# Kernel tuning notes

Hardware: AMD Instinct MI355X
Metric: run time of the kernel (lower is better)

## Reference

```python
import jax, jax.numpy as jnp
import numpy as np

B, T, S, U, VOCAB = 32, 64, 64, 512, 65


def setup_inputs() -> dict:
    key = jax.random.key(0)
    ks = jax.random.split(key, 16)
    sd = 0.05
    return {
        "shifted_labels": jax.random.randint(ks[0], (B, T), 0, VOCAB),
        "encoder_output": jax.random.normal(ks[1], (B, S, U), jnp.float32),
        "enc_state_h": jax.random.normal(ks[2], (B, U), jnp.float32),
        "enc_state_c": jax.random.normal(ks[3], (B, U), jnp.float32),
        # decoder LSTM params (keras gate order i,f,g,o)
        "Wx": jax.random.normal(ks[4], (VOCAB, 4 * U), jnp.float32) * sd,
        "Wh": jax.random.normal(ks[5], (U, 4 * U), jnp.float32) * sd,
        "b": jnp.zeros((4 * U,), jnp.float32),
        # Bahdanau attention params
        "W1": jax.random.normal(ks[6], (U, U), jnp.float32) * sd,
        "b1": jnp.zeros((U,), jnp.float32),
        "W2": jax.random.normal(ks[7], (U, U), jnp.float32) * sd,
        "b2": jnp.zeros((U,), jnp.float32),
        "V": jax.random.normal(ks[8], (U, 1), jnp.float32) * sd,
        "bv": jnp.zeros((1,), jnp.float32),
    }


def _lstm(xz, h0, c0, Wh):
    # xz: [B, T, 4U] precomputed input projections
    def step(carry, xz_t):
        h, c = carry
        z = xz_t + h @ Wh
        i, f, g, o = jnp.split(z, 4, axis=-1)
        c = jax.nn.sigmoid(f) * c + jax.nn.sigmoid(i) * jnp.tanh(g)
        h = jax.nn.sigmoid(o) * jnp.tanh(c)
        return (h, c), h

    (_, _), hs = jax.lax.scan(step, (h0, c0), jnp.swapaxes(xz, 0, 1))
    return jnp.swapaxes(hs, 0, 1)  # [B, T, U]


def reference(shifted_labels, encoder_output, enc_state_h, enc_state_c,
              Wx, Wh, b, W1, b1, W2, b2, V, bv):
    vocab = Wx.shape[0]
    x = jax.nn.one_hot(shifted_labels, vocab, dtype=encoder_output.dtype)  # [B,T,vocab]
    xz = jnp.einsum('btv,vk->btk', x, Wx) + b                              # [B,T,4U]
    dec = _lstm(xz, enc_state_h, enc_state_c, Wh)                          # [B,T,U]
    # Bahdanau attention, vectorized over all decoder timesteps at once
    d1 = dec @ W1 + b1                # [B,T,U]
    e2 = encoder_output @ W2 + b2     # [B,S,U]  (computed once, not per step)
    score = jnp.tanh(d1[:, :, None, :] + e2[:, None, :, :]) @ V + bv  # [B,T,S,1]
    w = jax.nn.softmax(score[..., 0], axis=-1)  # softmax over encoder positions S
    return jnp.transpose(w, (0, 2, 1))          # [B,S,T] (stack axis=2 in original)
```

## Files before the change

### kernel.cpp

```cpp
#include <hip/hip_runtime.h>
#include <hip/hip_bf16.h>


#define NB 32
#define NT 64
#define NS 64
#define NU 512
#define N4U 2048
#define NV 65
#define NWG 32

typedef unsigned int u32;
typedef __bf16 bf16_t;
typedef bf16_t bf16x8 __attribute__((ext_vector_type(8)));
typedef float f32x4 __attribute__((ext_vector_type(4)));
typedef u32 u32x4 __attribute__((ext_vector_type(4)));

__device__ __forceinline__ unsigned short f2bf(float f) {
  u32 u = __builtin_bit_cast(u32, f);
  u += 0x7fffu + ((u >> 16) & 1u);
  return (unsigned short)(u >> 16);
}
__device__ __forceinline__ float bf2f(unsigned short s) {
  return __builtin_bit_cast(float, (u32)s << 16);
}
__device__ __forceinline__ u32 pk2(float a, float b) {
  return (u32)f2bf(a) | ((u32)f2bf(b) << 16);
}
__device__ __forceinline__ float sigf(float x) { return 1.0f / (1.0f + __expf(-x)); }
__device__ __forceinline__ float tanhfast(float x) {
  float e = __expf(2.0f * x);
  return 1.0f - 2.0f / (e + 1.0f);
}

#define LOAD_HSLOT(DST, AP)                                                   \
  asm volatile(                                                               \
    "global_load_dwordx4 %0, %16, off sc0 sc1\n\t"                            \
    "global_load_dwordx4 %1, %16, off offset:64 sc0 sc1\n\t"                  \
    "global_load_dwordx4 %2, %16, off offset:128 sc0 sc1\n\t"                 \
    "global_load_dwordx4 %3, %16, off offset:192 sc0 sc1\n\t"                 \
    "global_load_dwordx4 %4, %16, off offset:256 sc0 sc1\n\t"                 \
    "global_load_dwordx4 %5, %16, off offset:320 sc0 sc1\n\t"                 \
    "global_load_dwordx4 %6, %16, off offset:384 sc0 sc1\n\t"                 \
    "global_load_dwordx4 %7, %16, off offset:448 sc0 sc1\n\t"                 \
    "global_load_dwordx4 %8, %16, off offset:512 sc0 sc1\n\t"                 \
    "global_load_dwordx4 %9, %16, off offset:576 sc0 sc1\n\t"                 \
    "global_load_dwordx4 %10, %16, off offset:640 sc0 sc1\n\t"                \
    "global_load_dwordx4 %11, %16, off offset:704 sc0 sc1\n\t"                \
    "global_load_dwordx4 %12, %16, off offset:768 sc0 sc1\n\t"                \
    "global_load_dwordx4 %13, %16, off offset:832 sc0 sc1\n\t"                \
    "global_load_dwordx4 %14, %16, off offset:896 sc0 sc1\n\t"                \
    "global_load_dwordx4 %15, %16, off offset:960 sc0 sc1\n\t"                \
    "s_waitcnt vmcnt(0)"                                                      \
    : "=&v"(DST[0]),  "=&v"(DST[1]),  "=&v"(DST[2]),  "=&v"(DST[3]),          \
      "=&v"(DST[4]),  "=&v"(DST[5]),  "=&v"(DST[6]),  "=&v"(DST[7]),          \
      "=&v"(DST[8]),  "=&v"(DST[9]),  "=&v"(DST[10]), "=&v"(DST[11]),         \
      "=&v"(DST[12]), "=&v"(DST[13]), "=&v"(DST[14]), "=&v"(DST[15])          \
    : "v"(AP)                                                                 \
    : "memory")

__global__ __launch_bounds__(256, 1)
void lstm_kernel(const int* __restrict__ labels,
                 const float* __restrict__ h0,
                 const float* __restrict__ c0,
                 const float* __restrict__ Wx,
                 const float* __restrict__ Wh,
                 const float* __restrict__ bias,
                 const float* __restrict__ enc,
                 const float* __restrict__ W2,
                 const float* __restrict__ b2,
                 const float* __restrict__ W1,
                 const float* __restrict__ b1,
                 u32* __restrict__ hbuf,
                 u32* __restrict__ flags,
                 unsigned short* __restrict__ d1_bf,
                 unsigned short* __restrict__ e2_bf)
{
  __shared__ float z_buf[NB][65];
  __shared__ float c_lds[NB][16];
  __shared__ float wx_lds[NV][65];
  __shared__ unsigned char lab_lds[NB * NT];

  const int tid  = threadIdx.x;
  const int g    = blockIdx.x;
  const int wave = tid >> 6, lane = tid & 63;
  const int l15  = lane & 15, l4 = lane >> 4;

  if (g >= NWG) {
    const int k = g - NWG;
    {
      const int r0 = k * 64 + wave * 16;
      const int arowE = r0 + l15;
      u32x4 afragE[16];
#pragma unroll
      for (int kt = 0; kt < 16; ++kt) {
        const float* ep = enc + arowE * NU + kt * 32 + l4 * 8;
        u32x4 t;
        t.x = pk2(ep[0], ep[1]); t.y = pk2(ep[2], ep[3]);
        t.z = pk2(ep[4], ep[5]); t.w = pk2(ep[6], ep[7]);
        afragE[kt] = t;
      }
      for (int cg = 0; cg < 8; ++cg) {
        f32x4 acc[4] = {};
        for (int kt = 0; kt < 16; ++kt) {
          bf16x8 a = __builtin_bit_cast(bf16x8, afragE[kt]);
          int k0 = kt * 32 + l4 * 8;
#pragma unroll
          for (int nt = 0; nt < 4; ++nt) {
            int col = cg * 64 + nt * 16 + l15;
            union { unsigned short us[8]; bf16x8 v; } bu;
#pragma unroll
            for (int e = 0; e < 8; ++e) bu.us[e] = f2bf(W2[(k0 + e) * NU + col]);
            acc[nt] = __builtin_amdgcn_mfma_f32_16x16x32_bf16(a, bu.v, acc[nt], 0, 0, 0);
          }
        }
#pragma unroll
        for (int nt = 0; nt < 4; ++nt) {
          int col = cg * 64 + nt * 16 + l15;
          float bc = b2[col];
#pragma unroll
          for (int ri = 0; ri < 4; ++ri)
            e2_bf[(r0 + l4 * 4 + ri) * NU + col] = f2bf(acc[nt][ri] + bc);
        }
      }
    }

    {
      const int wm = wave >> 1, wn = wave & 1;
      const int col = k * 16 + l15;
      const float bc1 = b1[col];
      bf16x8 bfrag1[16];
#pragma unroll
      for (int kt = 0; kt < 16; ++kt) {
        int kb = kt * 32 + l4 * 8;
        union { unsigned short us[8]; bf16x8 v; } bu;
#pragma unroll
        for (int e = 0; e < 8; ++e) bu.us[e] = f2bf(W1[(kb + e) * NU + col]);
        bfrag1[kt] = bu.v;
      }
      const int arow1 = wm * 16 + l15;
      for (int t = 1 + wn; t <= NT; t += 2) {
        {
          int guard = 0;
          for (;;) {
            u32 f = (u32)t;
            if (lane < NWG)
              f = __hip_atomic_load(flags + lane, __ATOMIC_RELAXED,
                                    __HIP_MEMORY_SCOPE_AGENT);
            if (__all(f >= (u32)t)) break;
            if (++guard > 2000000) break;
            __builtin_amdgcn_s_sleep(2);
          }
        }
        u32x4 hf[16];
        const u32* ap1 = hbuf + (size_t)t * 8192 + arow1 * 256 + l4 * 4;
        LOAD_HSLOT(hf, ap1);
        f32x4 acc = {0.f, 0.f, 0.f, 0.f};
#pragma unroll
        for (int kt = 0; kt < 16; ++kt)
          acc = __builtin_amdgcn_mfma_f32_16x16x32_bf16(
                  __builtin_bit_cast(bf16x8, hf[kt]), bfrag1[kt], acc, 0, 0, 0);
#pragma unroll
        for (int ri = 0; ri < 4; ++ri) {
          int b = wm * 16 + l4 * 4 + ri;
          d1_bf[(b * NT + (t - 1)) * NU + col] = f2bf(acc[ri] + bc1);
        }
      }
    }
    return;
  }

  const int wm = wave >> 1, wn = wave & 1;

  for (int i = tid; i < NV * 64; i += 256) {
    int v = i >> 6, c = i & 63;
    int j = (c >> 4) * NU + g * 16 + (c & 15);
    wx_lds[v][c] = Wx[v * N4U + j] + bias[j];
  }
  for (int i = tid; i < NB * 16; i += 256) {
    int r = i >> 4, u = i & 15;
    c_lds[r][u] = c0[r * NU + g * 16 + u];
  }
  for (int i = tid; i < NB * NT; i += 256) lab_lds[i] = (unsigned char)labels[i];

  bf16x8 bfrag[16][2];
#pragma unroll
  for (int kt = 0; kt < 16; ++kt) {
#pragma unroll
    for (int nt = 0; nt < 2; ++nt) {
      int c = wn * 32 + nt * 16 + l15;
      int j = (c >> 4) * NU + g * 16 + (c & 15);
      int kb = kt * 32 + l4 * 8;
      union { unsigned short us[8]; bf16x8 v; } bu;
#pragma unroll
      for (int e = 0; e < 8; ++e) bu.us[e] = f2bf(Wh[(kb + e) * N4U + j]);
      bfrag[kt][nt] = bu.v;
    }
  }

  const int arow = wm * 16 + l15;
  u32x4 afrag[16];
#pragma unroll
  for (int kt = 0; kt < 16; ++kt) {
    const float* hp = h0 + arow * NU + kt * 32 + l4 * 8;
    u32x4 t;
    t.x = pk2(hp[0], hp[1]); t.y = pk2(hp[2], hp[3]);
    t.z = pk2(hp[4], hp[5]); t.w = pk2(hp[6], hp[7]);
    afrag[kt] = t;
  }

  const int bb = tid >> 3;
  const int u2 = (tid & 7) * 2;
  const int ci = g * 8 + (tid & 7);

  for (int s = 0; s < NT; ++s) {
    f32x4 a00 = {0.f,0.f,0.f,0.f}, a01 = a00, a10 = a00, a11 = a00;
#pragma unroll
    for (int kt = 0; kt < 16; kt += 2) {
      bf16x8 av0 = __builtin_bit_cast(bf16x8, afrag[kt]);
      bf16x8 av1 = __builtin_bit_cast(bf16x8, afrag[kt + 1]);
      a00 = __builtin_amdgcn_mfma_f32_16x16x32_bf16(av0, bfrag[kt][0],     a00, 0, 0, 0);
      a10 = __builtin_amdgcn_mfma_f32_16x16x32_bf16(av0, bfrag[kt][1],     a10, 0, 0, 0);
      a01 = __builtin_amdgcn_mfma_f32_16x16x32_bf16(av1, bfrag[kt + 1][0], a01, 0, 0, 0);
      a11 = __builtin_amdgcn_mfma_f32_16x16x32_bf16(av1, bfrag[kt + 1][1], a11, 0, 0, 0);
    }
    f32x4 acc0 = a00 + a01, acc1 = a10 + a11;

#pragma unroll
    for (int ri = 0; ri < 4; ++ri) {
      z_buf[wm * 16 + l4 * 4 + ri][wn * 32 + l15]      = acc0[ri];
      z_buf[wm * 16 + l4 * 4 + ri][wn * 32 + 16 + l15] = acc1[ri];
    }
    __syncthreads();

    int lab = lab_lds[bb * NT + s];
    float hv[2];
#pragma unroll
    for (int q = 0; q < 2; ++q) {
      int u = u2 + q;
      float zi = z_buf[bb][u]      + wx_lds[lab][u];
      float zf = z_buf[bb][16 + u] + wx_lds[lab][16 + u];
      float zg = z_buf[bb][32 + u] + wx_lds[lab][32 + u];
      float zo = z_buf[bb][48 + u] + wx_lds[lab][48 + u];
      float cc = sigf(zf) * c_lds[bb][u] + sigf(zi) * tanhfast(zg);
      c_lds[bb][u] = cc;
      hv[q] = sigf(zo) * tanhfast(cc);
    }
    u32 pkv = pk2(hv[0], hv[1]);

    __hip_atomic_store(hbuf + (size_t)(s + 1) * 8192 + bb * 256 + ci, pkv,
                       __ATOMIC_RELAXED, __HIP_MEMORY_SCOPE_AGENT);

    asm volatile("s_waitcnt vmcnt(0)" ::: "memory");
    __syncthreads();

    if (tid == 0)
      __hip_atomic_store(flags + g, (u32)(s + 1),
                         __ATOMIC_RELAXED, __HIP_MEMORY_SCOPE_AGENT);

    if (s == NT - 1) break;

    {
      const u32 target = (u32)(s + 1);
      int guard = 0;
      for (;;) {
        u32 f = target;
        if (lane < NWG)
          f = __hip_atomic_load(flags + lane, __ATOMIC_RELAXED,
                                __HIP_MEMORY_SCOPE_AGENT);
        if (__all(f >= target)) break;
        if (++guard > 300000) break;
        __builtin_amdgcn_s_sleep(1);
      }
    }

    {
      const u32* ap = hbuf + (size_t)(s + 1) * 8192 + arow * 256 + l4 * 4;
      LOAD_HSLOT(afrag, ap);
    }
  }
}

__global__ __launch_bounds__(256, 1)
void score_kernel(const unsigned short* __restrict__ d1_bf,
                  const unsigned short* __restrict__ e2_bf,
                  const float* __restrict__ V,
                  float* __restrict__ out)
{
  const int tid = threadIdx.x;
  const int wave = tid >> 6, lane = tid & 63;
  const int p = blockIdx.x * 4 + wave;
  const int bb = p >> 6, t = p & 63;

  union { uint4 q; unsigned short us[8]; } dv;
  dv.q = *reinterpret_cast<const uint4*>(d1_bf + (bb * 64 + t) * NU + lane * 8);
  float d1f[8], Vf[8];
#pragma unroll
  for (int e = 0; e < 8; ++e) { d1f[e] = bf2f(dv.us[e]); Vf[e] = V[lane * 8 + e]; }

  float sc = 0.f;
  for (int s = 0; s < NS; ++s) {
    union { uint4 q; unsigned short us[8]; } ev;
    ev.q = *reinterpret_cast<const uint4*>(e2_bf + (bb * 64 + s) * NU + lane * 8);
    float part = 0.f;
#pragma unroll
    for (int e = 0; e < 8; ++e) part += tanhfast(d1f[e] + bf2f(ev.us[e])) * Vf[e];
#pragma unroll
    for (int o = 32; o > 0; o >>= 1) part += __shfl_xor(part, o);
    sc = (lane == s) ? part : sc;
  }
  float m = sc;
#pragma unroll
  for (int o = 32; o > 0; o >>= 1) m = fmaxf(m, __shfl_xor(m, o));
  float ex = __expf(sc - m);
  float sum = ex;
#pragma unroll
  for (int o = 32; o > 0; o >>= 1) sum += __shfl_xor(sum, o);
  out[(bb * 64 + lane) * 64 + t] = ex / sum;
}

extern "C" void kernel_launch(void* const* d_in, const int* in_sizes, int n_in,
                              void* d_out, int out_size, void* d_ws, size_t ws_size,
                              hipStream_t stream)
{
  (void)in_sizes; (void)n_in; (void)out_size;
  const int*   labels = (const int*)  d_in[0];
  const float* enc    = (const float*)d_in[1];
  const float* h0     = (const float*)d_in[2];
  const float* c0     = (const float*)d_in[3];
  const float* Wx     = (const float*)d_in[4];
  const float* Wh     = (const float*)d_in[5];
  const float* bias   = (const float*)d_in[6];
  const float* W1     = (const float*)d_in[7];
  const float* b1     = (const float*)d_in[8];
  const float* W2     = (const float*)d_in[9];
  const float* b2     = (const float*)d_in[10];
  const float* V      = (const float*)d_in[11];

  char* ws = (char*)d_ws;
  const size_t OFS_HB  = 32768;
  const size_t HB_SZ   = (size_t)65 * 8192 * 4;
  const size_t OFS_D1  = OFS_HB + HB_SZ;
  const size_t OFS_E2  = OFS_D1 + (2u << 20);
  if (ws_size < OFS_E2 + (2u << 20)) return;

  u32* flags = (u32*)(ws);
  u32* hbuf  = (u32*)(ws + OFS_HB);
  unsigned short* d1_bf = (unsigned short*)(ws + OFS_D1);
  unsigned short* e2_bf = (unsigned short*)(ws + OFS_E2);
  float* out = (float*)d_out;

  hipMemsetAsync(flags, 0, 256, stream);
  lstm_kernel<<<dim3(64), dim3(256), 0, stream>>>(labels, h0, c0, Wx, Wh, bias,
                                                  enc, W2, b2, W1, b1,
                                                  hbuf, flags, d1_bf, e2_bf);
  score_kernel<<<dim3(512), dim3(256), 0, stream>>>(d1_bf, e2_bf, V, out);
}
```

Before: 410.3 us.

## Defer W1 projection to after LSTM, pre-pack W1 to bf16 in prep kernel

```diff
diff --git a/kernel.cpp b/kernel.cpp
--- a/kernel.cpp
+++ b/kernel.cpp
@@ -60,6 +60,28 @@
     : "memory")
 
 __global__ __launch_bounds__(256, 1)
+void prep_kernel(const float* __restrict__ W1,
+                 unsigned short* __restrict__ w1bf,
+                 u32* __restrict__ flags)
+{
+  const int tid = threadIdx.x, g = blockIdx.x;
+  if (g == 0 && tid < 64) flags[tid] = 0;
+  int i0 = g * 8192 + tid;
+#pragma unroll
+  for (int j = 0; j < 32; ++j) {
+    int i = i0 + j * 256;
+    int e   = i & 7;
+    int l4  = (i >> 3) & 3;
+    int l15 = (i >> 5) & 15;
+    int c16 = (i >> 9) & 31;
+    int kt  = (i >> 14) & 15;
+    int k   = kt * 32 + l4 * 8 + e;
+    int col = c16 * 16 + l15;
+    w1bf[i] = f2bf(W1[k * NU + col]);
+  }
+}
+
+__global__ __launch_bounds__(256, 1)
 void lstm_kernel(const int* __restrict__ labels,
                  const float* __restrict__ h0,
                  const float* __restrict__ c0,
@@ -69,7 +91,7 @@
                  const float* __restrict__ enc,
                  const float* __restrict__ W2,
                  const float* __restrict__ b2,
-                 const float* __restrict__ W1,
+                 const unsigned short* __restrict__ w1bf,
                  const float* __restrict__ b1,
                  u32* __restrict__ hbuf,
                  u32* __restrict__ flags,
@@ -87,196 +109,209 @@
   const int l15  = lane & 15, l4 = lane >> 4;
 
   if (g >= NWG) {
-    const int k = g - NWG;
-    {
-      const int r0 = k * 64 + wave * 16;
-      const int arowE = r0 + l15;
-      u32x4 afragE[16];
-#pragma unroll
+    const int r0 = (g - NWG) * 64 + wave * 16;
+    const int arowE = r0 + l15;
+    u32x4 afragE[16];
+#pragma unroll
+    for (int kt = 0; kt < 16; ++kt) {
+      const float* ep = enc + arowE * NU + kt * 32 + l4 * 8;
+      u32x4 t;
+      t.x = pk2(ep[0], ep[1]); t.y = pk2(ep[2], ep[3]);
+      t.z = pk2(ep[4], ep[5]); t.w = pk2(ep[6], ep[7]);
+      afragE[kt] = t;
+    }
+    for (int cg = 0; cg < 8; ++cg) {
+      f32x4 acc[4] = {};
       for (int kt = 0; kt < 16; ++kt) {
-        const float* ep = enc + arowE * NU + kt * 32 + l4 * 8;
-        u32x4 t;
-        t.x = pk2(ep[0], ep[1]); t.y = pk2(ep[2], ep[3]);
-        t.z = pk2(ep[4], ep[5]); t.w = pk2(ep[6], ep[7]);
-        afragE[kt] = t;
-      }
-      for (int cg = 0; cg < 8; ++cg) {
-        f32x4 acc[4] = {};
-        for (int kt = 0; kt < 16; ++kt) {
-          bf16x8 a = __builtin_bit_cast(bf16x8, afragE[kt]);
-          int k0 = kt * 32 + l4 * 8;
-#pragma unroll
-          for (int nt = 0; nt < 4; ++nt) {
-            int col = cg * 64 + nt * 16 + l15;
-            union { unsigned short us[8]; bf16x8 v; } bu;
-#pragma unroll
-            for (int e = 0; e < 8; ++e) bu.us[e] = f2bf(W2[(k0 + e) * NU + col]);
-            acc[nt] = __builtin_amdgcn_mfma_f32_16x16x32_bf16(a, bu.v, acc[nt], 0, 0, 0);
-          }
-        }
+        bf16x8 a = __builtin_bit_cast(bf16x8, afragE[kt]);
+        int k0 = kt * 32 + l4 * 8;
 #pragma unroll
         for (int nt = 0; nt < 4; ++nt) {
           int col = cg * 64 + nt * 16 + l15;
-          float bc = b2[col];
-#pragma unroll
-          for (int ri = 0; ri < 4; ++ri)
-            e2_bf[(r0 + l4 * 4 + ri) * NU + col] = f2bf(acc[nt][ri] + bc);
+          union { unsigned short us[8]; bf16x8 v; } bu;
+#pragma unroll
+          for (int e = 0; e < 8; ++e) bu.us[e] = f2bf(W2[(k0 + e) * NU + col]);
+          acc[nt] = __builtin_amdgcn_mfma_f32_16x16x32_bf16(a, bu.v, acc[nt], 0, 0, 0);
         }
       }
-    }
-
-    {
-      const int wm = wave >> 1, wn = wave & 1;
-      const int col = k * 16 + l15;
-      const float bc1 = b1[col];
-      bf16x8 bfrag1[16];
-#pragma unroll
-      for (int kt = 0; kt < 16; ++kt) {
-        int kb = kt * 32 + l4 * 8;
-        union { unsigned short us[8]; bf16x8 v; } bu;
-#pragma unroll
-        for (int e = 0; e < 8; ++e) bu.us[e] = f2bf(W1[(kb + e) * NU + col]);
-        bfrag1[kt] = bu.v;
-      }
-      const int arow1 = wm * 16 + l15;
-      for (int t = 1 + wn; t <= NT; t += 2) {
-        {
-          int guard = 0;
-          for (;;) {
-            u32 f = (u32)t;
-            if (lane < NWG)
-              f = __hip_atomic_load(flags + lane, __ATOMIC_RELAXED,
-                                    __HIP_MEMORY_SCOPE_AGENT);
-            if (__all(f >= (u32)t)) break;
-            if (++guard > 2000000) break;
-            __builtin_amdgcn_s_sleep(2);
-          }
-        }
-        u32x4 hf[16];
-        const u32* ap1 = hbuf + (size_t)t * 8192 + arow1 * 256 + l4 * 4;
-        LOAD_HSLOT(hf, ap1);
-        f32x4 acc = {0.f, 0.f, 0.f, 0.f};
-#pragma unroll
-        for (int kt = 0; kt < 16; ++kt)
-          acc = __builtin_amdgcn_mfma_f32_16x16x32_bf16(
-                  __builtin_bit_cast(bf16x8, hf[kt]), bfrag1[kt], acc, 0, 0, 0);
-#pragma unroll
-        for (int ri = 0; ri < 4; ++ri) {
-          int b = wm * 16 + l4 * 4 + ri;
-          d1_bf[(b * NT + (t - 1)) * NU + col] = f2bf(acc[ri] + bc1);
-        }
-      }
-    }
-    return;
-  }
-
-  const int wm = wave >> 1, wn = wave & 1;
-
-  for (int i = tid; i < NV * 64; i += 256) {
-    int v = i >> 6, c = i & 63;
-    int j = (c >> 4) * NU + g * 16 + (c & 15);
-    wx_lds[v][c] = Wx[v * N4U + j] + bias[j];
-  }
-  for (int i = tid; i < NB * 16; i += 256) {
-    int r = i >> 4, u = i & 15;
-    c_lds[r][u] = c0[r * NU + g * 16 + u];
-  }
-  for (int i = tid; i < NB * NT; i += 256) lab_lds[i] = (unsigned char)labels[i];
-
-  bf16x8 bfrag[16][2];
-#pragma unroll
-  for (int kt = 0; kt < 16; ++kt) {
-#pragma unroll
-    for (int nt = 0; nt < 2; ++nt) {
-      int c = wn * 32 + nt * 16 + l15;
-      int j = (c >> 4) * NU + g * 16 + (c & 15);
-      int kb = kt * 32 + l4 * 8;
-      union { unsigned short us[8]; bf16x8 v; } bu;
-#pragma unroll
-      for (int e = 0; e < 8; ++e) bu.us[e] = f2bf(Wh[(kb + e) * N4U + j]);
-      bfrag[kt][nt] = bu.v;
-    }
-  }
-
-  const int arow = wm * 16 + l15;
-  u32x4 afrag[16];
-#pragma unroll
-  for (int kt = 0; kt < 16; ++kt) {
-    const float* hp = h0 + arow * NU + kt * 32 + l4 * 8;
-    u32x4 t;
-    t.x = pk2(hp[0], hp[1]); t.y = pk2(hp[2], hp[3]);
-    t.z = pk2(hp[4], hp[5]); t.w = pk2(hp[6], hp[7]);
-    afrag[kt] = t;
-  }
-
-  const int bb = tid >> 3;
-  const int u2 = (tid & 7) * 2;
-  const int ci = g * 8 + (tid & 7);
-
-  for (int s = 0; s < NT; ++s) {
-    f32x4 a00 = {0.f,0.f,0.f,0.f}, a01 = a00, a10 = a00, a11 = a00;
-#pragma unroll
-    for (int kt = 0; kt < 16; kt += 2) {
-      bf16x8 av0 = __builtin_bit_cast(bf16x8, afrag[kt]);
-      bf16x8 av1 = __builtin_bit_cast(bf16x8, afrag[kt + 1]);
-      a00 = __builtin_amdgcn_mfma_f32_16x16x32_bf16(av0, bfrag[kt][0],     a00, 0, 0, 0);
-      a10 = __builtin_amdgcn_mfma_f32_16x16x32_bf16(av0, bfrag[kt][1],     a10, 0, 0, 0);
-      a01 = __builtin_amdgcn_mfma_f32_16x16x32_bf16(av1, bfrag[kt + 1][0], a01, 0, 0, 0);
-      a11 = __builtin_amdgcn_mfma_f32_16x16x32_bf16(av1, bfrag[kt + 1][1], a11, 0, 0, 0);
-    }
-    f32x4 acc0 = a00 + a01, acc1 = a10 + a11;
-
-#pragma unroll
-    for (int ri = 0; ri < 4; ++ri) {
-      z_buf[wm * 16 + l4 * 4 + ri][wn * 32 + l15]      = acc0[ri];
-      z_buf[wm * 16 + l4 * 4 + ri][wn * 32 + 16 + l15] = acc1[ri];
-    }
-    __syncthreads();
-
-    int lab = lab_lds[bb * NT + s];
-    float hv[2];
-#pragma unroll
-    for (int q = 0; q < 2; ++q) {
-      int u = u2 + q;
-      float zi = z_buf[bb][u]      + wx_lds[lab][u];
-      float zf = z_buf[bb][16 + u] + wx_lds[lab][16 + u];
-      float zg = z_buf[bb][32 + u] + wx_lds[lab][32 + u];
-      float zo = z_buf[bb][48 + u] + wx_lds[lab][48 + u];
-      float cc = sigf(zf) * c_lds[bb][u] + sigf(zi) * tanhfast(zg);
-      c_lds[bb][u] = cc;
-      hv[q] = sigf(zo) * tanhfast(cc);
-    }
-    u32 pkv = pk2(hv[0], hv[1]);
-
-    __hip_atomic_store(hbuf + (size_t)(s + 1) * 8192 + bb * 256 + ci, pkv,
-                       __ATOMIC_RELAXED, __HIP_MEMORY_SCOPE_AGENT);
-
-    asm volatile("s_waitcnt vmcnt(0)" ::: "memory");
-    __syncthreads();
-
-    if (tid == 0)
-      __hip_atomic_store(flags + g, (u32)(s + 1),
-                         __ATOMIC_RELAXED, __HIP_MEMORY_SCOPE_AGENT);
-
-    if (s == NT - 1) break;
-
-    {
-      const u32 target = (u32)(s + 1);
+#pragma unroll
+      for (int nt = 0; nt < 4; ++nt) {
+        int col = cg * 64 + nt * 16 + l15;
+        float bc = b2[col];
+#pragma unroll
+        for (int ri = 0; ri < 4; ++ri)
+          e2_bf[(r0 + l4 * 4 + ri) * NU + col] = f2bf(acc[nt][ri] + bc);
+      }
+    }
+    if (wave == 0) {
       int guard = 0;
       for (;;) {
-        u32 f = target;
+        u32 f = 64;
         if (lane < NWG)
           f = __hip_atomic_load(flags + lane, __ATOMIC_RELAXED,
                                 __HIP_MEMORY_SCOPE_AGENT);
-        if (__all(f >= target)) break;
-        if (++guard > 300000) break;
+        if (__all(f >= 64u)) break;
+        if (++guard > 150000) break;
+        __builtin_amdgcn_s_sleep(127);
+      }
+    }
+  } else {
+    const int wm = wave >> 1, wn = wave & 1;
+
+    for (int i = tid; i < NV * 64; i += 256) {
+      int v = i >> 6, c = i & 63;
+      int j = (c >> 4) * NU + g * 16 + (c & 15);
+      wx_lds[v][c] = Wx[v * N4U + j] + bias[j];
+    }
+    for (int i = tid; i < NB * 16; i += 256) {
+      int r = i >> 4, u = i & 15;
+      c_lds[r][u] = c0[r * NU + g * 16 + u];
+    }
+    for (int i = tid; i < NB * NT; i += 256) lab_lds[i] = (unsigned char)labels[i];
+
+    bf16x8 bfrag[16][2];
+#pragma unroll
+    for (int kt = 0; kt < 16; ++kt) {
+#pragma unroll
+      for (int nt = 0; nt < 2; ++nt) {
+        int c = wn * 32 + nt * 16 + l15;
+        int j = (c >> 4) * NU + g * 16 + (c & 15);
+        int kb = kt * 32 + l4 * 8;
+        union { unsigned short us[8]; bf16x8 v; } bu;
+#pragma unroll
+        for (int e = 0; e < 8; ++e) bu.us[e] = f2bf(Wh[(kb + e) * N4U + j]);
+        bfrag[kt][nt] = bu.v;
+      }
+    }
+
+    const int arow = wm * 16 + l15;
+    u32x4 afrag[16];
+#pragma unroll
+    for (int kt = 0; kt < 16; ++kt) {
+      const float* hp = h0 + arow * NU + kt * 32 + l4 * 8;
+      u32x4 t;
+      t.x = pk2(hp[0], hp[1]); t.y = pk2(hp[2], hp[3]);
+      t.z = pk2(hp[4], hp[5]); t.w = pk2(hp[6], hp[7]);
+      afrag[kt] = t;
+    }
+
+    const int bb = tid >> 3;
+    const int u2 = (tid & 7) * 2;
+    const int ci = g * 8 + (tid & 7);
+
+    for (int s = 0; s < NT; ++s) {
+      f32x4 a00 = {0.f,0.f,0.f,0.f}, a01 = a00, a10 = a00, a11 = a00;
+#pragma unroll
+      for (int kt = 0; kt < 16; kt += 2) {
+        bf16x8 av0 = __builtin_bit_cast(bf16x8, afrag[kt]);
+        bf16x8 av1 = __builtin_bit_cast(bf16x8, afrag[kt + 1]);
+        a00 = __builtin_amdgcn_mfma_f32_16x16x32_bf16(av0, bfrag[kt][0],     a00, 0, 0, 0);
+        a10 = __builtin_amdgcn_mfma_f32_16x16x32_bf16(av0, bfrag[kt][1],     a10, 0, 0, 0);
+        a01 = __builtin_amdgcn_mfma_f32_16x16x32_bf16(av1, bfrag[kt + 1][0], a01, 0, 0, 0);
+        a11 = __builtin_amdgcn_mfma_f32_16x16x32_bf16(av1, bfrag[kt + 1][1], a11, 0, 0, 0);
+      }
+      f32x4 acc0 = a00 + a01, acc1 = a10 + a11;
+
+#pragma unroll
+      for (int ri = 0; ri < 4; ++ri) {
+        z_buf[wm * 16 + l4 * 4 + ri][wn * 32 + l15]      = acc0[ri];
+        z_buf[wm * 16 + l4 * 4 + ri][wn * 32 + 16 + l15] = acc1[ri];
+      }
+      __syncthreads();
+
+      int lab = lab_lds[bb * NT + s];
+      float hv[2];
+#pragma unroll
+      for (int q = 0; q < 2; ++q) {
+        int u = u2 + q;
+        float zi = z_buf[bb][u]      + wx_lds[lab][u];
+        float zf = z_buf[bb][16 + u] + wx_lds[lab][16 + u];
+        float zg = z_buf[bb][32 + u] + wx_lds[lab][32 + u];
+        float zo = z_buf[bb][48 + u] + wx_lds[lab][48 + u];
+        float cc = sigf(zf) * c_lds[bb][u] + sigf(zi) * tanhfast(zg);
+        c_lds[bb][u] = cc;
+        hv[q] = sigf(zo) * tanhfast(cc);
+      }
+      u32 pkv = pk2(hv[0], hv[1]);
+
+      __hip_atomic_store(hbuf + (size_t)(s + 1) * 8192 + bb * 256 + ci, pkv,
+                         __ATOMIC_RELAXED, __HIP_MEMORY_SCOPE_AGENT);
+
+      asm volatile("s_waitcnt vmcnt(0)" ::: "memory");
+      __syncthreads();
+
+      if (tid == 0)
+        __hip_atomic_store(flags + g, (u32)(s + 1),
+                           __ATOMIC_RELAXED, __HIP_MEMORY_SCOPE_AGENT);
+
+      if (s == NT - 1) break;
+
+      {
+        const u32 target = (u32)(s + 1);
+        int guard = 0;
+        for (;;) {
+          u32 f = target;
+          if (lane < NWG)
+            f = __hip_atomic_load(flags + lane, __ATOMIC_RELAXED,
+                                  __HIP_MEMORY_SCOPE_AGENT);
+          if (__all(f >= target)) break;
+          if (++guard > 300000) break;
+          __builtin_amdgcn_s_sleep(1);
+        }
+      }
+
+      {
+        const u32* ap = hbuf + (size_t)(s + 1) * 8192 + arow * 256 + l4 * 4;
+        LOAD_HSLOT(afrag, ap);
+      }
+    }
+
+    if (wave == 0) {
+      int guard = 0;
+      for (;;) {
+        u32 f = 64;
+        if (lane < NWG)
+          f = __hip_atomic_load(flags + lane, __ATOMIC_RELAXED,
+                                __HIP_MEMORY_SCOPE_AGENT);
+        if (__all(f >= 64u)) break;
+        if (++guard > 500000) break;
         __builtin_amdgcn_s_sleep(1);
       }
     }
-
-    {
-      const u32* ap = hbuf + (size_t)(s + 1) * 8192 + arow * 256 + l4 * 4;
-      LOAD_HSLOT(afrag, ap);
+  }
+
+  __syncthreads();
+
+  {
+    const int t = g + 1;
+    u32x4 A0[16], A1[16];
+    const u32* ap0 = hbuf + (size_t)t * 8192 + l15 * 256 + l4 * 4;
+    const u32* ap1 = hbuf + (size_t)t * 8192 + (16 + l15) * 256 + l4 * 4;
+    LOAD_HSLOT(A0, ap0);
+    LOAD_HSLOT(A1, ap1);
+
+#pragma unroll
+    for (int cg = 0; cg < 8; ++cg) {
+      const int c16 = wave * 8 + cg;
+      f32x4 acc0 = {0.f, 0.f, 0.f, 0.f}, acc1 = acc0;
+#pragma unroll
+      for (int kt = 0; kt < 16; ++kt) {
+        uint4 braw = *reinterpret_cast<const uint4*>(
+            w1bf + ((kt * 32 + c16) * 512 + l15 * 32 + l4 * 8));
+        bf16x8 b = __builtin_bit_cast(bf16x8, braw);
+        acc0 = __builtin_amdgcn_mfma_f32_16x16x32_bf16(
+                 __builtin_bit_cast(bf16x8, A0[kt]), b, acc0, 0, 0, 0);
+        acc1 = __builtin_amdgcn_mfma_f32_16x16x32_bf16(
+                 __builtin_bit_cast(bf16x8, A1[kt]), b, acc1, 0, 0, 0);
+      }
+      const int col = c16 * 16 + l15;
+      const float bc = b1[col];
+#pragma unroll
+      for (int ri = 0; ri < 4; ++ri) {
+        int b0 = l4 * 4 + ri;
+        d1_bf[((b0)      * NT + (t - 1)) * NU + col] = f2bf(acc0[ri] + bc);
+        d1_bf[((b0 + 16) * NT + (t - 1)) * NU + col] = f2bf(acc1[ri] + bc);
+      }
     }
   }
 }
@@ -338,21 +373,22 @@
   const float* V      = (const float*)d_in[11];
 
   char* ws = (char*)d_ws;
-  const size_t OFS_HB  = 32768;
-  const size_t HB_SZ   = (size_t)65 * 8192 * 4;
-  const size_t OFS_D1  = OFS_HB + HB_SZ;
+  const size_t OFS_W1B = 4096;
+  const size_t OFS_HB  = OFS_W1B + 524288;
+  const size_t OFS_D1  = OFS_HB + (size_t)65 * 32768;
   const size_t OFS_E2  = OFS_D1 + (2u << 20);
   if (ws_size < OFS_E2 + (2u << 20)) return;
 
   u32* flags = (u32*)(ws);
+  unsigned short* w1bf = (unsigned short*)(ws + OFS_W1B);
   u32* hbuf  = (u32*)(ws + OFS_HB);
   unsigned short* d1_bf = (unsigned short*)(ws + OFS_D1);
   unsigned short* e2_bf = (unsigned short*)(ws + OFS_E2);
   float* out = (float*)d_out;
 
-  hipMemsetAsync(flags, 0, 256, stream);
+  prep_kernel<<<dim3(32), dim3(256), 0, stream>>>(W1, w1bf, flags);
   lstm_kernel<<<dim3(64), dim3(256), 0, stream>>>(labels, h0, c0, Wx, Wh, bias,
-                                                  enc, W2, b2, W1, b1,
+                                                  enc, W2, b2, w1bf, b1,
                                                   hbuf, flags, d1_bf, e2_bf);
   score_kernel<<<dim3(512), dim3(256), 0, stream>>>(d1_bf, e2_bf, V, out);
 }
```

New measurement: 365.3 us. 1.12x faster.
